# Performance work log

Hardware: AMD Instinct MI355X
Metric: run time of the kernel (lower is better)

## Reference

```python
import jax, jax.numpy as jnp
import numpy as np

B = 8
D = 512        # d_hidn
H = 8          # n_head
DH = 64        # d_head
L = 6          # n_layer
DFF = 2048     # d_ff
GRID = 10
DMLP = 1024
NOUT = 1
EPS = 1e-6
CIN = 2048
SEQ = 1 + 24 * 32 + 9 * 12 + 5 * 7  # 912


def setup_inputs() -> dict:
    key = jax.random.key(0)
    ks = jax.random.split(key, 40)
    rn = lambda k, s, sc=0.02: jax.random.normal(k, s, jnp.float32) * sc
    inp = {
        "feat_dis_org": jax.random.normal(ks[0], (B, CIN, 24, 32), jnp.float32),
        "feat_dis_ref_1": jax.random.normal(ks[1], (B, CIN, 9, 12), jnp.float32),
        "feat_dis_ref_2": jax.random.normal(ks[2], (B, CIN, 5, 7), jnp.float32),
        "conv_w": rn(ks[3], (D, CIN)),
        "conv_b": rn(ks[4], (D,)),
        "scale_org_emb": jax.random.uniform(ks[5], (D,), jnp.float32),
        "ref_1_emb": jax.random.uniform(ks[6], (D,), jnp.float32),
        "ref_2_emb": rn(ks[7], (D,), 1.0),
        "pos_emb": rn(ks[8], (GRID, GRID, D), 0.02),
        "cls_token": rn(ks[9], (D,), 0.02),
        "Wq": rn(ks[10], (L, D, D)), "bq": rn(ks[11], (L, D)),
        "Wk": rn(ks[12], (L, D, D)), "bk": rn(ks[13], (L, D)),
        "Wv": rn(ks[14], (L, D, D)), "bv": rn(ks[15], (L, D)),
        "Wo": rn(ks[16], (L, D, D)), "bo": rn(ks[17], (L, D)),
        "ln1_g": jnp.ones((L, D), jnp.float32), "ln1_b": jnp.zeros((L, D), jnp.float32),
        "w1": rn(ks[18], (L, DFF, D)), "b1": rn(ks[19], (L, DFF)),
        "w2": rn(ks[20], (L, D, DFF)), "b2": rn(ks[21], (L, D)),
        "ln2_g": jnp.ones((L, D), jnp.float32), "ln2_b": jnp.zeros((L, D), jnp.float32),
        "proj_w1": rn(ks[22], (DMLP, D)),
        "proj_w2": rn(ks[23], (NOUT, DMLP)),
        "mask_inputs": jnp.ones((B, SEQ), jnp.int32),
    }
    return inp


def _ln(x, g, b):
    m = jnp.mean(x, -1, keepdims=True)
    v = jnp.mean((x - m) ** 2, -1, keepdims=True)
    return (x - m) * jax.lax.rsqrt(v + EPS) * g + b


def _embed(feat, chan_emb, conv_w, conv_b, pos_emb):
    # 1x1 conv (conv_enc) as a channel contraction: [b,2048,h,w] -> [b,D,h,w]
    x = jnp.einsum('bchw,dc->bdhw', feat, conv_w) + conv_b[None, :, None, None]
    x = x + chan_emb[None, :, None, None]           # scale/ref embedding
    h, w = x.shape[2], x.shape[3]
    # vectorized version of the nested-loop gather: t_i = int(i/h*Grid)
    ti = (jnp.arange(h) * GRID) // h
    tj = (jnp.arange(w) * GRID) // w
    sp = pos_emb[ti][:, tj]                          # [h,w,D]
    x = x + jnp.transpose(sp, (2, 0, 1))[None]       # [b,D,h,w]
    return jnp.transpose(x.reshape(x.shape[0], D, h * w), (0, 2, 1))  # [b,hw,D]


def reference(feat_dis_org, feat_dis_ref_1, feat_dis_ref_2, conv_w, conv_b,
              scale_org_emb, ref_1_emb, ref_2_emb, pos_emb, cls_token,
              Wq, bq, Wk, bk, Wv, bv, Wo, bo, ln1_g, ln1_b,
              w1, b1, w2, b2, ln2_g, ln2_b, proj_w1, proj_w2, mask_inputs):
    t_org = _embed(feat_dis_org, scale_org_emb, conv_w, conv_b, pos_emb)
    t_r1 = _embed(feat_dis_ref_1, ref_1_emb, conv_w, conv_b, pos_emb)
    t_r2 = _embed(feat_dis_ref_2, ref_2_emb, conv_w, conv_b, pos_emb)
    cls = jnp.broadcast_to(cls_token[None, None, :], (B, 1, D))
    x = jnp.concatenate([cls, t_org, t_r1, t_r2], axis=1)   # [B,SEQ,D]

    pad = (mask_inputs == 0)[:, None, None, :]              # [B,1,1,SEQ]
    scale = 1.0 / (DH ** 0.5)

    for i in range(L):
        s = x.shape[1]
        q = (x @ Wq[i].T + bq[i]).reshape(B, s, H, DH).transpose(0, 2, 1, 3)
        k = (x @ Wk[i].T + bk[i]).reshape(B, s, H, DH).transpose(0, 2, 1, 3)
        v = (x @ Wv[i].T + bv[i]).reshape(B, s, H, DH).transpose(0, 2, 1, 3)
        scores = jnp.einsum('bhqd,bhkd->bhqk', q, k) * scale
        scores = jnp.where(pad, -1e9, scores)
        prob = jax.nn.softmax(scores, axis=-1)
        ctx = jnp.einsum('bhqk,bhkd->bhqd', prob, v)
        ctx = ctx.transpose(0, 2, 1, 3).reshape(B, s, H * DH)
        att = ctx @ Wo[i].T + bo[i]
        x = _ln(x + att, ln1_g[i], ln1_b[i])
        ff = jax.nn.gelu(x @ w1[i].T + b1[i], approximate=False) @ w2[i].T + b2[i]
        x = _ln(x + ff, ln2_g[i], ln2_b[i])

    cls_out = x[:, 0, :]
    hmlp = jax.nn.gelu(cls_out @ proj_w1.T, approximate=False)
    pred = hmlp @ proj_w2.T                                   # [B,1]
    return pred
```

## Files before the change

### kernel.cpp

```cpp
#include <hip/hip_runtime.h>
#include <hip/hip_bf16.h>
#include <math.h>

#define SEQ 912
#define NTOK 911
#define CIN_ 2048
#define NLAYER 6

typedef _Float16 f16x8 __attribute__((ext_vector_type(8)));
typedef _Float16 f16x4 __attribute__((ext_vector_type(4)));
typedef float f32x4 __attribute__((ext_vector_type(4)));

__device__ __forceinline__ float gelu_f(float x) {
    float z = fabsf(x) * 0.70710678118654752f;
    float t = 1.0f / (1.0f + 0.3275911f * z);
    float poly = t * (0.254829592f +
                 t * (-0.284496736f +
                 t * (1.421413741f +
                 t * (-1.453152027f +
                 t * 1.061405429f))));
    float erfa = 1.0f - poly * __expf(-z * z);
    float erfv = copysignf(erfa, x);
    return 0.5f * x * (1.0f + erfv);
}

__device__ __forceinline__ int xcd_swizzle(int orig, int nwg) {
    int q = nwg >> 3, r = nwg & 7;
    int xcd = orig & 7, idx = orig >> 3;
    int base = (xcd < r) ? xcd * (q + 1) : r * (q + 1) + (xcd - r) * q;
    return base + idx;
}

__device__ __forceinline__ void gld16(const _Float16* g, _Float16* l) {
    __builtin_amdgcn_global_load_lds(
        (const __attribute__((address_space(1))) unsigned int*)g,
        (__attribute__((address_space(3))) unsigned int*)l,
        16, 0, 0);
}

__device__ __forceinline__ void stage_tile_g(const _Float16* Ab, const _Float16* Bb,
                                             size_t seg, _Float16* ldsW, int kk) {
    gld16(Ab + kk, ldsW);
    gld16(Ab + seg + kk, ldsW + 2048);
    gld16(Bb + kk, ldsW + 4096);
    gld16(Bb + seg + kk, ldsW + 6144);
}

__device__ __forceinline__ void compute_step_g(const _Float16* sb, int r0, int c0,
                                               int ln15, int quad, f32x4 (&acc)[4][4]) {
    f16x8 a[4], b[4];
#pragma unroll
    for (int i = 0; i < 4; ++i)
        a[i] = *(const f16x8*)&sb[(r0 + i * 16 + ln15) * 32 + quad * 8];
#pragma unroll
    for (int j = 0; j < 4; ++j)
        b[j] = *(const f16x8*)&sb[4096 + (c0 + j * 16 + ln15) * 32 + quad * 8];
#pragma unroll
    for (int i = 0; i < 4; ++i)
#pragma unroll
        for (int j = 0; j < 4; ++j)
            acc[i][j] = __builtin_amdgcn_mfma_f32_16x16x32_f16(a[i], b[j], acc[i][j], 0, 0, 0);
}

template <int ACT, int QKV>
__global__ __launch_bounds__(256) void gemm16(
    const _Float16* __restrict__ A, const _Float16* __restrict__ B,
    const float* __restrict__ bias, _Float16* __restrict__ Cout,
    _Float16* __restrict__ vT, int M, int N, int K, int ldc)
{
    __shared__ __align__(16) _Float16 smem[4 * 8192];
    _Float16* Cs = smem;
    const int t = threadIdx.x;
    const int nbx = N >> 7;
    const int swz = xcd_swizzle(blockIdx.x, gridDim.x);
    const int by = swz / nbx, bx = swz - by * nbx;
    const int m0 = by * 128, n0 = bx * 128;
    const int lane = t & 63, w = t >> 6;
    const int r0 = (w >> 1) * 64, c0 = (w & 1) * 64;
    const int ln15 = lane & 15, quad = lane >> 4;

    f32x4 zero = {0.f, 0.f, 0.f, 0.f};
    f32x4 acc[4][4];
#pragma unroll
    for (int i = 0; i < 4; ++i)
#pragma unroll
        for (int j = 0; j < 4; ++j) acc[i][j] = zero;

    const _Float16* Ab = A + (size_t)(m0 + w * 16 + (lane >> 2)) * K + (lane & 3) * 8;
    const _Float16* Bb = B + (size_t)(n0 + w * 16 + (lane >> 2)) * K + (lane & 3) * 8;
    const size_t seg = (size_t)64 * K;
    _Float16* ldsW = smem + w * 512;

    const int nK = K >> 5;
    stage_tile_g(Ab, Bb, seg, ldsW, 0);
    stage_tile_g(Ab, Bb, seg, ldsW + 8192, 32);

    for (int s = 0; s < nK - 2; ++s) {
        stage_tile_g(Ab, Bb, seg, ldsW + ((s + 2) & 3) * 8192, (s + 2) << 5);
        asm volatile("s_waitcnt vmcnt(8)" ::: "memory");
        __builtin_amdgcn_s_barrier();
        __builtin_amdgcn_sched_barrier(0);
        compute_step_g(smem + (s & 3) * 8192, r0, c0, ln15, quad, acc);
    }
    asm volatile("s_waitcnt vmcnt(4)" ::: "memory");
    __builtin_amdgcn_s_barrier();
    __builtin_amdgcn_sched_barrier(0);
    compute_step_g(smem + ((nK - 2) & 3) * 8192, r0, c0, ln15, quad, acc);
    asm volatile("s_waitcnt vmcnt(0)" ::: "memory");
    __builtin_amdgcn_s_barrier();
    __builtin_amdgcn_sched_barrier(0);
    compute_step_g(smem + ((nK - 1) & 3) * 8192, r0, c0, ln15, quad, acc);

    if (QKV && n0 >= 1024) {
#pragma unroll
        for (int j = 0; j < 4; ++j) {
            int gn = n0 + c0 + j * 16 + ln15;
            float bv = bias[gn];
            int chan = gn - 1024;
            int hh = chan >> 6, d = chan & 63;
#pragma unroll
            for (int i = 0; i < 4; ++i) {
                int gmBase = m0 + r0 + i * 16 + quad * 4;
                int bb = gmBase / 912, s = gmBase - bb * 912;
                f16x4 hv4;
#pragma unroll
                for (int r = 0; r < 4; ++r) hv4[r] = (_Float16)(acc[i][j][r] + bv);
                *(f16x4*)&vT[((size_t)((bb * 8 + hh) * 64 + d)) * 960 + s] = hv4;
            }
        }
    } else {
        __syncthreads();
#pragma unroll
        for (int half = 0; half < 2; ++half) {
            if ((w >> 1) == half) {
#pragma unroll
                for (int j = 0; j < 4; ++j) {
                    float bv = bias[n0 + c0 + j * 16 + ln15];
#pragma unroll
                    for (int i = 0; i < 4; ++i)
#pragma unroll
                        for (int r = 0; r < 4; ++r) {
                            float val = acc[i][j][r] + bv;
                            if (ACT == 1) val = gelu_f(val);
                            Cs[(i * 16 + quad * 4 + r) * 136 + c0 + j * 16 + ln15] = (_Float16)val;
                        }
                }
            }
            __syncthreads();
#pragma unroll
            for (int uu = 0; uu < 4; ++uu) {
                int u = t + uu * 256;
                int lr = u >> 4, ch = (u & 15) * 8;
                int gm = m0 + half * 64 + lr;
                if (gm < M)
                    *(f16x8*)&Cout[(size_t)gm * ldc + n0 + ch] = *(const f16x8*)&Cs[lr * 136 + ch];
            }
            __syncthreads();
        }
    }
}

__device__ __forceinline__ void stage_tile_s(const _Float16* Ab, const _Float16* Bb,
                                             size_t seg, _Float16* ldsW, int kk) {
    gld16(Ab + kk, ldsW);
    gld16(Ab + seg + kk, ldsW + 2048);
    gld16(Bb + kk, ldsW + 4096);
}

__device__ __forceinline__ void compute_step_s(const _Float16* sb, int r0, int c0,
                                               int ln15, int quad, f32x4 (&acc)[4][2]) {
    f16x8 a[4], b[2];
#pragma unroll
    for (int i = 0; i < 4; ++i)
        a[i] = *(const f16x8*)&sb[(r0 + i * 16 + ln15) * 32 + quad * 8];
#pragma unroll
    for (int j = 0; j < 2; ++j)
        b[j] = *(const f16x8*)&sb[4096 + (c0 + j * 16 + ln15) * 32 + quad * 8];
#pragma unroll
    for (int i = 0; i < 4; ++i)
#pragma unroll
        for (int j = 0; j < 2; ++j)
            acc[i][j] = __builtin_amdgcn_mfma_f32_16x16x32_f16(a[i], b[j], acc[i][j], 0, 0, 0);
}

__global__ __launch_bounds__(256) void gemm16_p32(
    const _Float16* __restrict__ A, const _Float16* __restrict__ B,
    float* __restrict__ out, int M, int N, int K)
{
    __shared__ __align__(16) _Float16 smem[3 * 6144];
    const int t = threadIdx.x;
    const int nbx = N >> 6;
    const int swz = xcd_swizzle(blockIdx.x, gridDim.x);
    const int by = swz / nbx, bx = swz - by * nbx;
    const int m0 = by * 128, n0 = bx * 64;
    const int lane = t & 63, w = t >> 6;
    const int r0 = (w >> 1) * 64, c0 = (w & 1) * 32;
    const int ln15 = lane & 15, quad = lane >> 4;

    f32x4 zero = {0.f, 0.f, 0.f, 0.f};
    f32x4 acc[4][2];
#pragma unroll
    for (int i = 0; i < 4; ++i)
#pragma unroll
        for (int j = 0; j < 2; ++j) acc[i][j] = zero;

    const _Float16* Ab = A + (size_t)(m0 + w * 16 + (lane >> 2)) * K + (lane & 3) * 8;
    const _Float16* Bb = B + (size_t)(n0 + w * 16 + (lane >> 2)) * K + (lane & 3) * 8;
    const size_t seg = (size_t)64 * K;
    _Float16* ldsW = smem + w * 512;

    const int nK = K >> 5;
    stage_tile_s(Ab, Bb, seg, ldsW, 0);
    stage_tile_s(Ab, Bb, seg, ldsW + 6144, 32);

    for (int s = 0; s < nK - 2; ++s) {
        asm volatile("s_waitcnt vmcnt(3)" ::: "memory");
        __builtin_amdgcn_s_barrier();
        __builtin_amdgcn_sched_barrier(0);
        stage_tile_s(Ab, Bb, seg, ldsW + ((s + 2) % 3) * 6144, (s + 2) << 5);
        compute_step_s(smem + (s % 3) * 6144, r0, c0, ln15, quad, acc);
    }
    asm volatile("s_waitcnt vmcnt(3)" ::: "memory");
    __builtin_amdgcn_s_barrier();
    __builtin_amdgcn_sched_barrier(0);
    compute_step_s(smem + ((nK - 2) % 3) * 6144, r0, c0, ln15, quad, acc);
    asm volatile("s_waitcnt vmcnt(0)" ::: "memory");
    __builtin_amdgcn_s_barrier();
    __builtin_amdgcn_sched_barrier(0);
    compute_step_s(smem + ((nK - 1) % 3) * 6144, r0, c0, ln15, quad, acc);

#pragma unroll
    for (int j = 0; j < 2; ++j) {
        int gn = n0 + c0 + j * 16 + ln15;
#pragma unroll
        for (int i = 0; i < 4; ++i) {
            int gmBase = m0 + r0 + i * 16 + quad * 4;
#pragma unroll
            for (int r = 0; r < 4; ++r) {
                int gm = gmBase + r;
                if (gm < M) out[(size_t)gm * N + gn] = acc[i][j][r];
            }
        }
    }
}

__global__ __launch_bounds__(256) void cast16_kernel(
    const float* __restrict__ src, _Float16* __restrict__ dst, int n4)
{
    int i = blockIdx.x * 256 + threadIdx.x;
    if (i < n4) {
        float4 v = ((const float4*)src)[i];
        f16x4 h;
        h[0] = (_Float16)v.x; h[1] = (_Float16)v.y;
        h[2] = (_Float16)v.z; h[3] = (_Float16)v.w;
        ((f16x4*)dst)[i] = h;
    }
}

__global__ __launch_bounds__(256) void cast2_kernel(
    const float* __restrict__ s1, _Float16* __restrict__ d1, int n4_1,
    const float* __restrict__ s2, _Float16* __restrict__ d2, int n4_2)
{
    int i = blockIdx.x * 256 + threadIdx.x;
    if (i < n4_1) {
        float4 v = ((const float4*)s1)[i];
        f16x4 h;
        h[0] = (_Float16)v.x; h[1] = (_Float16)v.y;
        h[2] = (_Float16)v.z; h[3] = (_Float16)v.w;
        ((f16x4*)d1)[i] = h;
    } else {
        int j = i - n4_1;
        if (j < n4_2) {
            float4 v = ((const float4*)s2)[j];
            f16x4 h;
            h[0] = (_Float16)v.x; h[1] = (_Float16)v.y;
            h[2] = (_Float16)v.z; h[3] = (_Float16)v.w;
            ((f16x4*)d2)[j] = h;
        }
    }
}

__global__ __launch_bounds__(256) void pack_qkvw_kernel(
    const float* __restrict__ Wq, const float* __restrict__ Wk,
    const float* __restrict__ Wv, _Float16* __restrict__ dst)
{
    int idx = blockIdx.x * 256 + threadIdx.x;
    if (idx >= 6 * 1536 * 128) return;
    int c4 = idx & 127;
    int rc = idx >> 7;
    int r = rc % 1536;
    int l = rc / 1536;
    const float* src = (r < 512) ? Wq : (r < 1024) ? Wk : Wv;
    float4 v = *(const float4*)(src + ((size_t)l * 512 + (r & 511)) * 512 + c4 * 4);
    f16x4 h;
    h[0] = (_Float16)v.x; h[1] = (_Float16)v.y;
    h[2] = (_Float16)v.z; h[3] = (_Float16)v.w;
    *(f16x4*)(dst + ((size_t)l * 1536 + r) * 512 + c4 * 4) = h;
}

__global__ __launch_bounds__(256) void pack_qkvb_kernel(
    const float* __restrict__ bq, const float* __restrict__ bk,
    const float* __restrict__ bv, float* __restrict__ dst)
{
    int idx = blockIdx.x * 256 + threadIdx.x;
    if (idx < 6 * 1536) {
        int r = idx % 1536, l = idx / 1536;
        const float* s = (r < 512) ? bq : (r < 1024) ? bk : bv;
        dst[idx] = s[l * 512 + (r & 511)];
    }
}

__global__ __launch_bounds__(256) void transpose_feat_kernel(
    const float* __restrict__ feat, _Float16* __restrict__ patch, int HW, int tok_off)
{
    __shared__ float tile[32][33];
    const int b = blockIdx.z;
    const int c0 = blockIdx.y * 32;
    const int p0 = blockIdx.x * 32;
    const int tx = threadIdx.x, ty = threadIdx.y;
#pragma unroll
    for (int i = 0; i < 4; ++i) {
        int c = c0 + ty + i * 8;
        int p = p0 + tx;
        tile[ty + i * 8][tx] = (p < HW) ? feat[((size_t)b * CIN_ + c) * HW + p] : 0.f;
    }
    __syncthreads();
#pragma unroll
    for (int i = 0; i < 4; ++i) {
        int p = p0 + ty + i * 8;
        int c = c0 + tx;
        if (p < HW)
            patch[((size_t)(b * NTOK + tok_off + p)) * CIN_ + c] = (_Float16)tile[tx][ty + i * 8];
    }
}

__global__ __launch_bounds__(128) void build_x_red(
    const float* __restrict__ part, const float* __restrict__ conv_b,
    const float* __restrict__ cls_token,
    const float* __restrict__ emb_org, const float* __restrict__ emb_r1,
    const float* __restrict__ emb_r2, const float* __restrict__ pos_emb,
    float* __restrict__ x, _Float16* __restrict__ x16)
{
    const int row = blockIdx.x;
    const int b = row / SEQ;
    const int tt = row - b * SEQ;
    const int d4 = threadIdx.x;
    float4 o;
    if (tt == 0) {
        o = ((const float4*)cls_token)[d4];
    } else {
        int tp = tt - 1;
        const float* ce; int hh, ww, p;
        if (tp < 768)      { p = tp;       hh = 24; ww = 32; ce = emb_org; }
        else if (tp < 876) { p = tp - 768; hh = 9;  ww = 12; ce = emb_r1; }
        else               { p = tp - 876; hh = 5;  ww = 7;  ce = emb_r2; }
        int i = p / ww, j = p - i * ww;
        int ti = (i * 10) / hh, tj = (j * 10) / ww;
        size_t prow = (size_t)(b * NTOK + tp) * 512;
        float4 t0 = ((const float4*)(part + prow))[d4];
        float4 cb = ((const float4*)conv_b)[d4];
        float4 cv = ((const float4*)ce)[d4];
        float4 pv = ((const float4*)(pos_emb + (size_t)(ti * 10 + tj) * 512))[d4];
        o.x = t0.x + cb.x + cv.x + pv.x;
        o.y = t0.y + cb.y + cv.y + pv.y;
        o.z = t0.z + cb.z + cv.z + pv.z;
        o.w = t0.w + cb.w + cv.w + pv.w;
    }
    ((float4*)(x + (size_t)row * 512))[d4] = o;
    f16x4 h;
    h[0] = (_Float16)o.x; h[1] = (_Float16)o.y;
    h[2] = (_Float16)o.z; h[3] = (_Float16)o.w;
    ((f16x4*)(x16 + (size_t)row * 512))[d4] = h;
}

__global__ __launch_bounds__(64) void ln_residual_red(
    float* __restrict__ x, _Float16* __restrict__ x16,
    const float* __restrict__ part, const float* __restrict__ bias,
    const float* __restrict__ g, const float* __restrict__ bta)
{
    const int row = blockIdx.x;
    const int t = threadIdx.x;
    float4* xr = (float4*)(x + (size_t)row * 512);
    const float4* p0 = (const float4*)(part + (size_t)row * 512);
    const float4* bb = (const float4*)bias;
    float4 a0 = xr[t], a1 = xr[t + 64];
    float4 q0 = p0[t], q1 = p0[t + 64];
    float4 c0 = bb[t], c1 = bb[t + 64];
    a0.x += q0.x + c0.x; a0.y += q0.y + c0.y;
    a0.z += q0.z + c0.z; a0.w += q0.w + c0.w;
    a1.x += q1.x + c1.x; a1.y += q1.y + c1.y;
    a1.z += q1.z + c1.z; a1.w += q1.w + c1.w;
    float s = a0.x + a0.y + a0.z + a0.w + a1.x + a1.y + a1.z + a1.w;
#pragma unroll
    for (int o = 32; o; o >>= 1) s += __shfl_xor(s, o, 64);
    const float mean = s * (1.f / 512.f);
    float sq = 0.f;
    sq += (a0.x - mean) * (a0.x - mean); sq += (a0.y - mean) * (a0.y - mean);
    sq += (a0.z - mean) * (a0.z - mean); sq += (a0.w - mean) * (a0.w - mean);
    sq += (a1.x - mean) * (a1.x - mean); sq += (a1.y - mean) * (a1.y - mean);
    sq += (a1.z - mean) * (a1.z - mean); sq += (a1.w - mean) * (a1.w - mean);
#pragma unroll
    for (int o = 32; o; o >>= 1) sq += __shfl_xor(sq, o, 64);
    const float rstd = rsqrtf(sq * (1.f / 512.f) + 1e-6f);
    const float4 g0 = ((const float4*)g)[t], g1 = ((const float4*)g)[t + 64];
    const float4 e0 = ((const float4*)bta)[t], e1 = ((const float4*)bta)[t + 64];
    float4 o0, o1;
    o0.x = (a0.x - mean) * rstd * g0.x + e0.x;
    o0.y = (a0.y - mean) * rstd * g0.y + e0.y;
    o0.z = (a0.z - mean) * rstd * g0.z + e0.z;
    o0.w = (a0.w - mean) * rstd * g0.w + e0.w;
    o1.x = (a1.x - mean) * rstd * g1.x + e1.x;
    o1.y = (a1.y - mean) * rstd * g1.y + e1.y;
    o1.z = (a1.z - mean) * rstd * g1.z + e1.z;
    o1.w = (a1.w - mean) * rstd * g1.w + e1.w;
    xr[t] = o0; xr[t + 64] = o1;
    f16x4 h0, h1;
    h0[0] = (_Float16)o0.x; h0[1] = (_Float16)o0.y;
    h0[2] = (_Float16)o0.z; h0[3] = (_Float16)o0.w;
    h1[0] = (_Float16)o1.x; h1[1] = (_Float16)o1.y;
    h1[2] = (_Float16)o1.z; h1[3] = (_Float16)o1.w;
    f16x4* xh = (f16x4*)(x16 + (size_t)row * 512);
    xh[t] = h0; xh[t + 64] = h1;
}

__global__ __launch_bounds__(256) void attn_mfma(
    const _Float16* __restrict__ qk, const _Float16* __restrict__ vT,
    const int* __restrict__ mask, _Float16* __restrict__ ctx)
{
    __shared__ __align__(16) _Float16 Ks[64 * 72];
    __shared__ __align__(16) _Float16 VTs[64 * 72];
    __shared__ __align__(16) _Float16 Pw[4][16 * 72];
    __shared__ float biasS[64];
    const int swz = xcd_swizzle(blockIdx.x, 960);
    const int qt = swz % 15;
    const int hb = swz / 15;
    const int h = hb & 7, b = hb >> 3;
    const int q0 = qt * 64;
    const int t = threadIdx.x;
    const int wave = t >> 6, lane = t & 63;
    const int ln15 = lane & 15, quad = lane >> 4;
    const int qrow = q0 + wave * 16 + ln15;

    f16x8 qf[2];
#pragma unroll
    for (int ks = 0; ks < 2; ++ks) {
        f16x8 z = {0, 0, 0, 0, 0, 0, 0, 0};
        qf[ks] = (qrow < SEQ)
            ? *(const f16x8*)(qk + (size_t)(b * SEQ + qrow) * 1024 + h * 64 + ks * 32 + quad * 8)
            : z;
    }

    f32x4 oacc[4];
    f32x4 zero = {0.f, 0.f, 0.f, 0.f};
#pragma unroll
    for (int dj = 0; dj < 4; ++dj) oacc[dj] = zero;
    float m_i = -1e30f, l_i = 0.f;

    for (int kb = 0; kb < 960; kb += 64) {
#pragma unroll
        for (int i = 0; i < 2; ++i) {
            int u = t + i * 256;
            int r = u >> 3, ch = (u & 7) * 8;
            int kg = kb + r;
            f16x8 kvv = {0, 0, 0, 0, 0, 0, 0, 0};
            if (kg < SEQ) kvv = *(const f16x8*)(qk + (size_t)(b * SEQ + kg) * 1024 + 512 + h * 64 + ch);
            *(f16x8*)&Ks[r * 72 + ch] = kvv;
            f16x8 vv = {0, 0, 0, 0, 0, 0, 0, 0};
            if (kb + ch < SEQ)
                vv = *(const f16x8*)(vT + ((size_t)((b * 8 + h) * 64 + r)) * 960 + kb + ch);
            *(f16x8*)&VTs[r * 72 + ch] = vv;
        }
        if (t < 64) {
            int kg = kb + t;
            biasS[t] = (kg < SEQ) ? (mask[b * SEQ + kg] ? 0.f : -1e9f) : -2e9f;
        }
        __syncthreads();

        f32x4 st[4];
#pragma unroll
        for (int jj = 0; jj < 4; ++jj) st[jj] = zero;
#pragma unroll
        for (int jj = 0; jj < 4; ++jj)
#pragma unroll
            for (int ks = 0; ks < 2; ++ks) {
                f16x8 kf = *(const f16x8*)&Ks[(jj * 16 + ln15) * 72 + ks * 32 + quad * 8];
                st[jj] = __builtin_amdgcn_mfma_f32_16x16x32_f16(kf, qf[ks], st[jj], 0, 0, 0);
            }

        float p[4][4];
        float mloc = -3e38f;
#pragma unroll
        for (int jj = 0; jj < 4; ++jj) {
            f32x4 bfr = *(const f32x4*)&biasS[jj * 16 + quad * 4];
#pragma unroll
            for (int r = 0; r < 4; ++r) {
                float sv = st[jj][r] * 0.125f + bfr[r];
                p[jj][r] = sv;
                mloc = fmaxf(mloc, sv);
            }
        }
        mloc = fmaxf(mloc, __shfl_xor(mloc, 16, 64));
        mloc = fmaxf(mloc, __shfl_xor(mloc, 32, 64));
        float mnew = fmaxf(m_i, mloc);
        float alpha = __expf(m_i - mnew);
        m_i = mnew;
        float sloc = 0.f;
#pragma unroll
        for (int jj = 0; jj < 4; ++jj)
#pragma unroll
            for (int r = 0; r < 4; ++r) {
                p[jj][r] = __expf(p[jj][r] - mnew);
                sloc += p[jj][r];
            }
        sloc += __shfl_xor(sloc, 16, 64);
        sloc += __shfl_xor(sloc, 32, 64);
        l_i = l_i * alpha + sloc;

        float ar[4];
#pragma unroll
        for (int r = 0; r < 4; ++r) ar[r] = __shfl(alpha, quad * 4 + r, 64);
#pragma unroll
        for (int dj = 0; dj < 4; ++dj)
#pragma unroll
            for (int r = 0; r < 4; ++r) oacc[dj][r] *= ar[r];

        _Float16* pw = &Pw[wave][0];
#pragma unroll
        for (int jj = 0; jj < 4; ++jj)
#pragma unroll
            for (int r = 0; r < 4; ++r)
                pw[ln15 * 72 + jj * 16 + quad * 4 + r] = (_Float16)p[jj][r];
        f16x8 pf[2];
#pragma unroll
        for (int ks = 0; ks < 2; ++ks)
            pf[ks] = *(const f16x8*)&pw[ln15 * 72 + ks * 32 + quad * 8];

#pragma unroll
        for (int dj = 0; dj < 4; ++dj)
#pragma unroll
            for (int ks = 0; ks < 2; ++ks) {
                f16x8 vf = *(const f16x8*)&VTs[(dj * 16 + ln15) * 72 + ks * 32 + quad * 8];
                oacc[dj] = __builtin_amdgcn_mfma_f32_16x16x32_f16(pf[ks], vf, oacc[dj], 0, 0, 0);
            }
        __syncthreads();
    }

    float linv[4];
#pragma unroll
    for (int r = 0; r < 4; ++r) linv[r] = 1.f / __shfl(l_i, quad * 4 + r, 64);
#pragma unroll
    for (int dj = 0; dj < 4; ++dj)
#pragma unroll
        for (int r = 0; r < 4; ++r) {
            int row = q0 + wave * 16 + quad * 4 + r;
            if (row < SEQ)
                ctx[(size_t)(b * SEQ + row) * 512 + h * 64 + dj * 16 + ln15] =
                    (_Float16)(oacc[dj][r] * linv[r]);
        }
}

__global__ __launch_bounds__(64) void head1_kernel(
    const float* __restrict__ x, const float* __restrict__ w,
    float* __restrict__ hmlp)
{
    const int n = blockIdx.x & 1023;
    const int b = blockIdx.x >> 10;
    const int t = threadIdx.x;
    const float4* cls = (const float4*)(x + (size_t)b * SEQ * 512);
    const float4* wr = (const float4*)(w + (size_t)n * 512);
    float s = 0.f;
#pragma unroll
    for (int i = 0; i < 2; ++i) {
        float4 a = cls[t + i * 64], c = wr[t + i * 64];
        s += a.x * c.x + a.y * c.y + a.z * c.z + a.w * c.w;
    }
#pragma unroll
    for (int o = 32; o; o >>= 1) s += __shfl_xor(s, o, 64);
    if (t == 0) hmlp[b * 1024 + n] = gelu_f(s);
}

__global__ __launch_bounds__(256) void head2_kernel(
    const float* __restrict__ hmlp, const float* __restrict__ w,
    float* __restrict__ out)
{
    __shared__ float red[4];
    const int b = blockIdx.x;
    const int t = threadIdx.x;
    float s = 0.f;
    for (int i = t; i < 1024; i += 256) s += hmlp[b * 1024 + i] * w[i];
#pragma unroll
    for (int o = 32; o; o >>= 1) s += __shfl_xor(s, o, 64);
    if ((t & 63) == 0) red[t >> 6] = s;
    __syncthreads();
    if (t == 0) out[b] = red[0] + red[1] + red[2] + red[3];
}

extern "C" void kernel_launch(void* const* d_in, const int* in_sizes, int n_in,
                              void* d_out, int out_size, void* d_ws, size_t ws_size,
                              hipStream_t stream)
{
    const float* feat_org = (const float*)d_in[0];
    const float* feat_r1  = (const float*)d_in[1];
    const float* feat_r2  = (const float*)d_in[2];
    const float* conv_w   = (const float*)d_in[3];
    const float* conv_b   = (const float*)d_in[4];
    const float* emb_org  = (const float*)d_in[5];
    const float* emb_r1   = (const float*)d_in[6];
    const float* emb_r2   = (const float*)d_in[7];
    const float* pos_emb  = (const float*)d_in[8];
    const float* cls_tok  = (const float*)d_in[9];
    const float* Wq = (const float*)d_in[10];
    const float* bq = (const float*)d_in[11];
    const float* Wk = (const float*)d_in[12];
    const float* bk = (const float*)d_in[13];
    const float* Wv = (const float*)d_in[14];
    const float* bv = (const float*)d_in[15];
    const float* Wo = (const float*)d_in[16];
    const float* bo = (const float*)d_in[17];
    const float* ln1g = (const float*)d_in[18];
    const float* ln1b = (const float*)d_in[19];
    const float* w1 = (const float*)d_in[20];
    const float* b1 = (const float*)d_in[21];
    const float* w2 = (const float*)d_in[22];
    const float* b2 = (const float*)d_in[23];
    const float* ln2g = (const float*)d_in[24];
    const float* ln2b = (const float*)d_in[25];
    const float* pw1 = (const float*)d_in[26];
    const float* pw2 = (const float*)d_in[27];
    const int*   mask = (const int*)d_in[28];

    char* base = (char*)d_ws;
    _Float16* ffh16 = (_Float16*)base;
    _Float16* patch16 = ffh16;
    base += (size_t)7296 * 2048 * 2;
    float* x = (float*)base; base += (size_t)7296 * 512 * 4;
    _Float16* qk16 = (_Float16*)base; base += (size_t)7296 * 1024 * 2;
    _Float16* vT16 = (_Float16*)base; base += (size_t)8 * 8 * 64 * 960 * 2;
    _Float16* ctx16 = (_Float16*)base; base += (size_t)7296 * 512 * 2;
    _Float16* x16   = (_Float16*)base; base += (size_t)7296 * 512 * 2;
    _Float16* wqkv_all = (_Float16*)base; base += (size_t)6 * 1536 * 512 * 2;
    _Float16* wo_all   = (_Float16*)base; base += (size_t)6 * 512 * 512 * 2;
    _Float16* w1_l16   = (_Float16*)base; base += (size_t)2048 * 512 * 2;
    _Float16* w2_l16   = (_Float16*)base; base += (size_t)512 * 2048 * 2;
    float* bqkv_all = (float*)base; base += 6 * 1536 * 4;
    float* hmlp = (float*)base; base += 8 * 1024 * 4;

    float* partO = (float*)ffh16;
    float* partF = (float*)qk16;
    _Float16* convw16 = x16;

    dim3 tb(32, 8);
    hipLaunchKernelGGL(transpose_feat_kernel, dim3(24, 64, 8), tb, 0, stream,
                       feat_org, patch16, 768, 0);
    hipLaunchKernelGGL(transpose_feat_kernel, dim3(4, 64, 8), tb, 0, stream,
                       feat_r1, patch16, 108, 768);
    hipLaunchKernelGGL(transpose_feat_kernel, dim3(2, 64, 8), tb, 0, stream,
                       feat_r2, patch16, 35, 876);
    hipLaunchKernelGGL(cast16_kernel, dim3(1024), 256, 0, stream,
                       conv_w, convw16, 512 * 2048 / 4);
    hipLaunchKernelGGL(cast16_kernel, dim3(1536), 256, 0, stream,
                       Wo, wo_all, 6 * 512 * 512 / 4);
    hipLaunchKernelGGL(pack_qkvw_kernel, dim3(4608), 256, 0, stream,
                       Wq, Wk, Wv, wqkv_all);
    hipLaunchKernelGGL(pack_qkvb_kernel, dim3(36), 256, 0, stream,
                       bq, bk, bv, bqkv_all);

    hipLaunchKernelGGL(gemm16_p32, dim3(456), 256, 0, stream,
                       patch16, convw16, partF, 7288, 512, 2048);
    hipLaunchKernelGGL(build_x_red, dim3(7296), 128, 0, stream,
                       partF, conv_b, cls_tok, emb_org, emb_r1, emb_r2, pos_emb, x, x16);

    for (int l = 0; l < NLAYER; ++l) {
        hipLaunchKernelGGL(cast2_kernel, dim3(2048), 256, 0, stream,
                           w1 + (size_t)l * 2048 * 512, w1_l16, 2048 * 512 / 4,
                           w2 + (size_t)l * 512 * 2048, w2_l16, 512 * 2048 / 4);
        hipLaunchKernelGGL((gemm16<0, 1>), dim3(684), 256, 0, stream,
                           x16, wqkv_all + (size_t)l * 1536 * 512, bqkv_all + l * 1536,
                           qk16, vT16, 7296, 1536, 512, 1024);
        hipLaunchKernelGGL(attn_mfma, dim3(960), 256, 0, stream,
                           qk16, vT16, mask, ctx16);
        hipLaunchKernelGGL(gemm16_p32, dim3(456), 256, 0, stream,
                           ctx16, wo_all + (size_t)l * 512 * 512, partO, 7296, 512, 512);
        hipLaunchKernelGGL(ln_residual_red, dim3(7296), 64, 0, stream,
                           x, x16, partO, bo + l * 512, ln1g + l * 512, ln1b + l * 512);
        hipLaunchKernelGGL((gemm16<1, 0>), dim3(912), 256, 0, stream,
                           x16, w1_l16, b1 + l * 2048,
                           ffh16, (_Float16*)nullptr, 7296, 2048, 512, 2048);
        hipLaunchKernelGGL(gemm16_p32, dim3(456), 256, 0, stream,
                           ffh16, w2_l16, partF, 7296, 512, 2048);
        hipLaunchKernelGGL(ln_residual_red, dim3(7296), 64, 0, stream,
                           x, x16, partF, b2 + l * 512, ln2g + l * 512, ln2b + l * 512);
    }

    hipLaunchKernelGGL(head1_kernel, dim3(8 * 1024), 64, 0, stream, x, pw1, hmlp);
    hipLaunchKernelGGL(head2_kernel, dim3(8), 256, 0, stream, hmlp, pw2, (float*)d_out);
}
```

Baseline: 1.300 ms.

## Double-buffer attention K/V tiles and keep P in registers via key permutation

The attention kernel now double-buffers K, V^T and mask-bias tiles in shared memory, prefetching the next tile into registers while the current one is computed, which leaves one barrier per iteration instead of two. Key rows are loaded in a permuted order so the S accumulator layout matches the MFMA A-operand layout for P·V. That lets P be packed straight from registers and removes the per-wave LDS round trip. Softmax switches to exp2 with the log2e factor folded into the scale and mask bias. The cost is more shared memory and registers, and the permutation has to line up exactly with the MFMA operand layouts.

Measured after the change: 1.507 ms. 16.0% more time.

```diff
diff --git a/kernel.cpp b/kernel.cpp
--- a/kernel.cpp
+++ b/kernel.cpp
@@ -427,10 +427,9 @@
     const _Float16* __restrict__ qk, const _Float16* __restrict__ vT,
     const int* __restrict__ mask, _Float16* __restrict__ ctx)
 {
-    __shared__ __align__(16) _Float16 Ks[64 * 72];
-    __shared__ __align__(16) _Float16 VTs[64 * 72];
-    __shared__ __align__(16) _Float16 Pw[4][16 * 72];
-    __shared__ float biasS[64];
+    __shared__ __align__(16) _Float16 Ks[2][64 * 72];
+    __shared__ __align__(16) _Float16 VTs[2][64 * 72];
+    __shared__ float biasS[2][64];
     const int swz = xcd_swizzle(blockIdx.x, 960);
     const int qt = swz % 15;
     const int hb = swz / 15;
@@ -441,6 +440,18 @@
     const int ln15 = lane & 15, quad = lane >> 4;
     const int qrow = q0 + wave * 16 + ln15;
 
+    int r_[2], ch_[2], klog_[2];
+    const _Float16 *kp_[2], *vp_[2];
+#pragma unroll
+    for (int i = 0; i < 2; ++i) {
+        int u = t + i * 256;
+        r_[i] = u >> 3; ch_[i] = (u & 7) * 8;
+        klog_[i] = (r_[i] & 0x23) | ((r_[i] & 0x0C) << 1) | ((r_[i] & 0x10) >> 2);
+        kp_[i] = qk + (size_t)(b * SEQ + klog_[i]) * 1024 + 512 + h * 64 + ch_[i];
+        vp_[i] = vT + ((size_t)((b * 8 + h) * 64 + r_[i])) * 960 + ch_[i];
+    }
+    const int klog_b = (t & 0x23) | ((t & 0x0C) << 1) | ((t & 0x10) >> 2);
+
     f16x8 qf[2];
 #pragma unroll
     for (int ks = 0; ks < 2; ++ks) {
@@ -456,25 +467,41 @@
     for (int dj = 0; dj < 4; ++dj) oacc[dj] = zero;
     float m_i = -1e30f, l_i = 0.f;
 
-    for (int kb = 0; kb < 960; kb += 64) {
+    f16x8 kreg[2], vreg[2];
+    float breg = 0.f;
+#pragma unroll
+    for (int i = 0; i < 2; ++i) {
+        f16x8 z = {0, 0, 0, 0, 0, 0, 0, 0};
+        kreg[i] = (klog_[i] < SEQ) ? *(const f16x8*)kp_[i] : z;
+        vreg[i] = (ch_[i] < SEQ) ? *(const f16x8*)vp_[i] : z;
+    }
+    if (t < 64) {
+        breg = (klog_b < SEQ) ? (mask[b * SEQ + klog_b] ? 0.f : -1.442695e9f) : -2.9e9f;
+    }
+
+    const float SC = 0.125f * 1.44269504f;
+    for (int it = 0; it < 15; ++it) {
+        const int buf = it & 1;
 #pragma unroll
         for (int i = 0; i < 2; ++i) {
-            int u = t + i * 256;
-            int r = u >> 3, ch = (u & 7) * 8;
-            int kg = kb + r;
-            f16x8 kvv = {0, 0, 0, 0, 0, 0, 0, 0};
-            if (kg < SEQ) kvv = *(const f16x8*)(qk + (size_t)(b * SEQ + kg) * 1024 + 512 + h * 64 + ch);
-            *(f16x8*)&Ks[r * 72 + ch] = kvv;
-            f16x8 vv = {0, 0, 0, 0, 0, 0, 0, 0};
-            if (kb + ch < SEQ)
-                vv = *(const f16x8*)(vT + ((size_t)((b * 8 + h) * 64 + r)) * 960 + kb + ch);
-            *(f16x8*)&VTs[r * 72 + ch] = vv;
-        }
-        if (t < 64) {
-            int kg = kb + t;
-            biasS[t] = (kg < SEQ) ? (mask[b * SEQ + kg] ? 0.f : -1e9f) : -2e9f;
-        }
+            *(f16x8*)&Ks[buf][r_[i] * 72 + ch_[i]] = kreg[i];
+            *(f16x8*)&VTs[buf][r_[i] * 72 + ch_[i]] = vreg[i];
+        }
+        if (t < 64) biasS[buf][t] = breg;
         __syncthreads();
+        if (it + 1 < 15) {
+            const int kb = (it + 1) * 64;
+#pragma unroll
+            for (int i = 0; i < 2; ++i) {
+                f16x8 z = {0, 0, 0, 0, 0, 0, 0, 0};
+                kreg[i] = (kb + klog_[i] < SEQ) ? *(const f16x8*)(kp_[i] + (size_t)kb * 1024) : z;
+                vreg[i] = (kb + ch_[i] < SEQ) ? *(const f16x8*)(vp_[i] + kb) : z;
+            }
+            if (t < 64) {
+                int kg = kb + klog_b;
+                breg = (kg < SEQ) ? (mask[b * SEQ + kg] ? 0.f : -1.442695e9f) : -2.9e9f;
+            }
+        }
 
         f32x4 st[4];
 #pragma unroll
@@ -483,7 +510,7 @@
         for (int jj = 0; jj < 4; ++jj)
 #pragma unroll
             for (int ks = 0; ks < 2; ++ks) {
-                f16x8 kf = *(const f16x8*)&Ks[(jj * 16 + ln15) * 72 + ks * 32 + quad * 8];
+                f16x8 kf = *(const f16x8*)&Ks[buf][(jj * 16 + ln15) * 72 + ks * 32 + quad * 8];
                 st[jj] = __builtin_amdgcn_mfma_f32_16x16x32_f16(kf, qf[ks], st[jj], 0, 0, 0);
             }
 
@@ -491,10 +518,10 @@
         float mloc = -3e38f;
 #pragma unroll
         for (int jj = 0; jj < 4; ++jj) {
-            f32x4 bfr = *(const f32x4*)&biasS[jj * 16 + quad * 4];
+            f32x4 bfr = *(const f32x4*)&biasS[buf][jj * 16 + quad * 4];
 #pragma unroll
             for (int r = 0; r < 4; ++r) {
-                float sv = st[jj][r] * 0.125f + bfr[r];
+                float sv = st[jj][r] * SC + bfr[r];
                 p[jj][r] = sv;
                 mloc = fmaxf(mloc, sv);
             }
@@ -502,14 +529,14 @@
         mloc = fmaxf(mloc, __shfl_xor(mloc, 16, 64));
         mloc = fmaxf(mloc, __shfl_xor(mloc, 32, 64));
         float mnew = fmaxf(m_i, mloc);
-        float alpha = __expf(m_i - mnew);
+        float alpha = exp2f(m_i - mnew);
         m_i = mnew;
         float sloc = 0.f;
 #pragma unroll
         for (int jj = 0; jj < 4; ++jj)
 #pragma unroll
             for (int r = 0; r < 4; ++r) {
-                p[jj][r] = __expf(p[jj][r] - mnew);
+                p[jj][r] = exp2f(p[jj][r] - mnew);
                 sloc += p[jj][r];
             }
         sloc += __shfl_xor(sloc, 16, 64);
@@ -524,25 +551,25 @@
 #pragma unroll
             for (int r = 0; r < 4; ++r) oacc[dj][r] *= ar[r];
 
-        _Float16* pw = &Pw[wave][0];
-#pragma unroll
-        for (int jj = 0; jj < 4; ++jj)
-#pragma unroll
-            for (int r = 0; r < 4; ++r)
-                pw[ln15 * 72 + jj * 16 + quad * 4 + r] = (_Float16)p[jj][r];
         f16x8 pf[2];
 #pragma unroll
-        for (int ks = 0; ks < 2; ++ks)
-            pf[ks] = *(const f16x8*)&pw[ln15 * 72 + ks * 32 + quad * 8];
+        for (int ks = 0; ks < 2; ++ks) {
+            f16x8 v;
+#pragma unroll
+            for (int r = 0; r < 4; ++r) {
+                v[r]     = (_Float16)p[2 * ks][r];
+                v[4 + r] = (_Float16)p[2 * ks + 1][r];
+            }
+            pf[ks] = v;
+        }
 
 #pragma unroll
         for (int dj = 0; dj < 4; ++dj)
 #pragma unroll
             for (int ks = 0; ks < 2; ++ks) {
-                f16x8 vf = *(const f16x8*)&VTs[(dj * 16 + ln15) * 72 + ks * 32 + quad * 8];
+                f16x8 vf = *(const f16x8*)&VTs[buf][(dj * 16 + ln15) * 72 + ks * 32 + quad * 8];
                 oacc[dj] = __builtin_amdgcn_mfma_f32_16x16x32_f16(pf[ks], vf, oacc[dj], 0, 0, 0);
             }
-        __syncthreads();
     }
 
     float linv[4];
```
